# Performance work log

Hardware: AMD Instinct MI355X
Metric: run time of the kernel (lower is better)

Reference implementation:

```python
import jax, jax.numpy as jnp
import numpy as np

N_E, E_DIM = 1024, 256

def setup_inputs() -> dict:
    key = jax.random.key(0)
    k1, k2 = jax.random.split(key)
    z = jax.random.normal(k1, (16, E_DIM, 64, 64), dtype=jnp.float32)
    codebook = jax.random.normal(k2, (N_E, E_DIM), dtype=jnp.float32)
    return {"z": z, "codebook": codebook}

def reference(z, codebook):
    B, C, H, W = z.shape  # C == e_dim
    zp = jnp.transpose(z, (0, 2, 3, 1))          # B,H,W,C
    zf = zp.reshape(-1, C)                        # N,C with N=B*H*W
    # L2 distance: ||z||^2 + ||c||^2 - 2 z c^T  -> [N, n_e]
    d = (jnp.sum(zf * zf, axis=1, keepdims=True)
         + jnp.sum(codebook * codebook, axis=1)
         - 2.0 * jnp.matmul(zf, codebook.T))
    idx = jnp.argmin(d, axis=1)                   # [N] int
    # one-hot @ codebook == gather (same math)
    z_q = codebook[idx].reshape(zp.shape)         # B,H,W,C
    codebook_loss = jnp.mean((z_q - jax.lax.stop_gradient(zp)) ** 2)
    z_q_out = jnp.transpose(z_q, (0, 3, 1, 2))    # B,C,H,W
    min_encoding_indices = idx.reshape(B, 1, H, W)
    return (z_q_out, codebook_loss, jnp.zeros((), z_q_out.dtype), min_encoding_indices)
```

## Files before the change

kernel.cpp:

```cpp
#include <hip/hip_runtime.h>

#define HW 4096
#define NE 1024
#define LOSS_OFF 16777216
#define IDX_OFF  16777218
#define MARGIN 0.08f

typedef __attribute__((ext_vector_type(8))) _Float16 half8v;
typedef __attribute__((ext_vector_type(4))) float float4v;

#define WS_LIST_OFF   64
#define WS_CNORM_OFF  262208
#define WS_CBH_OFF    266304
#define WS_PART_OFF   790592

__device__ __forceinline__ unsigned short f16rne(float f) {
    _Float16 h = (_Float16)f;
    return __builtin_bit_cast(unsigned short, h);
}

__device__ __forceinline__ unsigned f16pk(float a, float b) {
    auto h = __builtin_amdgcn_cvt_pkrtz(a, b);
    return __builtin_bit_cast(unsigned, h);
}

__device__ __forceinline__ void stage16(const void* g, void* l) {
    __builtin_amdgcn_global_load_lds(
        (const __attribute__((address_space(1))) unsigned*)g,
        (__attribute__((address_space(3))) unsigned*)l, 16, 0, 0);
}

__global__ __launch_bounds__(256) void k0_prep(const float* __restrict__ cb,
                                               float* __restrict__ cnorm,
                                               unsigned short* __restrict__ cbh,
                                               int* __restrict__ flagcnt) {
    const int tid = threadIdx.x;
    if (blockIdx.x == 0 && tid == 0) *flagcnt = 0;
    const int e = blockIdx.x * 64 + (tid >> 2);
    const int j = tid & 3;
    const float4* src = (const float4*)(cb + (size_t)e * 256 + j * 64);
    unsigned short* dst = cbh + (size_t)e * 256 + j * 64;
    float s = 0.f;
#pragma unroll
    for (int i = 0; i < 16; ++i) {
        float4 v = src[i];
        s += v.x * v.x + v.y * v.y + v.z * v.z + v.w * v.w;
        unsigned p0 = (unsigned)f16rne(v.x) | ((unsigned)f16rne(v.y) << 16);
        unsigned p1 = (unsigned)f16rne(v.z) | ((unsigned)f16rne(v.w) << 16);
        *(uint2*)(dst + i * 4) = make_uint2(p0, p1);
    }
    s += __shfl_xor(s, 1, 64);
    s += __shfl_xor(s, 2, 64);
    if (j == 0) cnorm[e] = 0.5f * s;
}

__global__ __launch_bounds__(256) void k1_mfma(const float* __restrict__ z,
                                               const unsigned short* __restrict__ cbh,
                                               const float* __restrict__ cnorm,
                                               float* __restrict__ out_idx,
                                               int* __restrict__ flagcnt,
                                               int* __restrict__ flaglist) {
    __shared__ __align__(16) char smem[67072];
    float* cand1 = (float*)(smem + 65536);
    int*   candi = (int*)  (smem + 66048);
    float* cand2 = (float*)(smem + 66560);

    const int tid = threadIdx.x;
    const int lane = tid & 63, wid = tid >> 6;
    const int wx = wid & 1, wy = wid >> 1;
    const int lr = lane & 15, lg = lane >> 4;

    const int n0 = blockIdx.x * 64;
    const int hw0 = n0 & 4095;
    const float* zb = z + (size_t)(n0 >> 12) * (256 * HW);
    const char* cbh_b = (const char*)cbh;

    {
        const int row = tid & 63, kg8 = tid >> 6;
        const unsigned zswz = (unsigned)((row & 15) << 4);
#pragma unroll
        for (int it = 0; it < 8; ++it) {
            int kb = (kg8 + it * 4) * 8;
            float v[8];
#pragma unroll
            for (int q = 0; q < 8; ++q) v[q] = zb[(size_t)(kb + q) * HW + hw0 + row];
            unsigned pk[4];
#pragma unroll
            for (int q = 0; q < 4; ++q) pk[q] = f16pk(v[2*q], v[2*q+1]);
            unsigned scol = (unsigned)(kb * 2) ^ zswz;
            *(int4*)(smem + row * 512 + scol) = make_int4(pk[0], pk[1], pk[2], pk[3]);
        }
    }
    __syncthreads();

    half8v A[2][8];
#pragma unroll
    for (int mi = 0; mi < 2; ++mi)
#pragma unroll
        for (int ks = 0; ks < 8; ++ks)
            A[mi][ks] = *(const half8v*)(smem + (32*wy + 16*mi + lr) * 512
                                              + ((unsigned)(64*ks + 16*lg) ^ (unsigned)(lr << 4)));
    __syncthreads();

    char* mybuf0 = smem + wid * 8192;
    char* mybuf1 = smem + 32768 + wid * 8192;
    const int el      = (lane >> 5);
    const unsigned c0 = (unsigned)((lane & 31) * 16);
    const size_t  eb0 = (size_t)wx * 512;

#pragma unroll
    for (int i = 0; i < 8; ++i) {
        int e_loc = 2 * i + el;
        unsigned col = c0 ^ (unsigned)((e_loc & 15) << 4);
        stage16(cbh_b + (eb0 + e_loc) * 512 + col, mybuf0 + i * 1024);
    }

    const float* cnp = cnorm + wx * 512 + lr;
    float b1[8], b2[8]; int bi[8];
#pragma unroll
    for (int i = 0; i < 8; ++i) { b1[i] = 1e30f; b2[i] = 1e30f; bi[i] = 0; }

    for (int c = 0; c < 32; ++c) {
        char* cur = (c & 1) ? mybuf1 : mybuf0;
        if (c < 31) {
            char* nb = (c & 1) ? mybuf0 : mybuf1;
            const size_t ebase = eb0 + (size_t)(c + 1) * 16;
#pragma unroll
            for (int i = 0; i < 8; ++i) {
                int e_loc = 2 * i + el;
                unsigned col = c0 ^ (unsigned)((e_loc & 15) << 4);
                stage16(cbh_b + (ebase + e_loc) * 512 + col, nb + i * 1024);
            }
            asm volatile("s_waitcnt vmcnt(8)" ::: "memory");
        } else {
            asm volatile("s_waitcnt vmcnt(0)" ::: "memory");
        }
        __builtin_amdgcn_sched_barrier(0);

        const char* bp = cur + lr * 512;
        float4v a0 = {0.f,0.f,0.f,0.f}, a1 = a0;
#pragma unroll
        for (int ks = 0; ks < 8; ++ks) {
            half8v B = *(const half8v*)(bp + ((unsigned)(64*ks + 16*lg) ^ (unsigned)(lr << 4)));
            a0 = __builtin_amdgcn_mfma_f32_16x16x32_f16(A[0][ks], B, a0, 0, 0, 0);
            a1 = __builtin_amdgcn_mfma_f32_16x16x32_f16(A[1][ks], B, a1, 0, 0, 0);
        }

        const float cn = cnp[c * 16];
        const int e = wx * 512 + c * 16 + lr;
#pragma unroll
        for (int r = 0; r < 4; ++r) {
            float s0 = cn - a0[r];
            b2[r] = fminf(b2[r], fmaxf(b1[r], s0));
            if (s0 < b1[r]) { b1[r] = s0; bi[r] = e; }
            float s1 = cn - a1[r];
            b2[4+r] = fminf(b2[4+r], fmaxf(b1[4+r], s1));
            if (s1 < b1[4+r]) { b1[4+r] = s1; bi[4+r] = e; }
        }
    }

#pragma unroll
    for (int m = 1; m <= 8; m <<= 1) {
#pragma unroll
        for (int s = 0; s < 8; ++s) {
            float o1 = __shfl_xor(b1[s], m, 64);
            float o2 = __shfl_xor(b2[s], m, 64);
            int   oi = __shfl_xor(bi[s], m, 64);
            float m2 = fminf(fmaxf(b1[s], o1), fminf(b2[s], o2));
            if (o1 < b1[s] || (o1 == b1[s] && oi < bi[s])) { b1[s] = o1; bi[s] = oi; }
            b2[s] = m2;
        }
    }
    if (lr == 0) {
#pragma unroll
        for (int mi = 0; mi < 2; ++mi)
#pragma unroll
            for (int r = 0; r < 4; ++r) {
                int row = 32 * wy + 16 * mi + 4 * lg + r;
                cand1[row * 2 + wx] = b1[mi * 4 + r];
                cand2[row * 2 + wx] = b2[mi * 4 + r];
                candi[row * 2 + wx] = bi[mi * 4 + r];
            }
    }
    __syncthreads();
    if (tid < 64) {
        float s1a = cand1[tid * 2], s1b = cand1[tid * 2 + 1];
        int   ia = candi[tid * 2],  ib = candi[tid * 2 + 1];
        float s2 = fminf(fminf(cand2[tid * 2], cand2[tid * 2 + 1]), fmaxf(s1a, s1b));
        float s1; int iw;
        if (s1b < s1a || (s1b == s1a && ib < ia)) { s1 = s1b; iw = ib; }
        else { s1 = s1a; iw = ia; }
        out_idx[n0 + tid] = (float)iw;
        if (s2 - s1 < MARGIN) {
            int p = atomicAdd(flagcnt, 1);
            flaglist[p] = n0 + tid;
        }
    }
}

__global__ __launch_bounds__(256) void k1b_refine(const float* __restrict__ z,
                                                  const float* __restrict__ cb,
                                                  const float* __restrict__ cnorm,
                                                  const int* __restrict__ flagcnt,
                                                  const int* __restrict__ flaglist,
                                                  float* __restrict__ out_idx) {
    __shared__ float zr[4][260];
    __shared__ int   rows[4];
    __shared__ float wb[4][4];
    __shared__ int   wi[4][4];
    const int tid = threadIdx.x;
    const int lane = tid & 63, w = tid >> 6;
    const int gid = tid >> 2, j = tid & 3;
    const int count = *flagcnt;
    for (int base = blockIdx.x * 4; base < count; base += gridDim.x * 4) {
        const int nr = min(4, count - base);
        __syncthreads();
        if (tid < nr) rows[tid] = flaglist[base + tid];
        __syncthreads();
        for (int r = 0; r < nr; ++r) {
            const int n = rows[r];
            zr[r][tid] = z[((size_t)(n >> 12) * 256 + tid) * HW + (n & 4095)];
        }
        __syncthreads();

        float acc[16][4];
#pragma unroll
        for (int p = 0; p < 16; ++p)
#pragma unroll
            for (int r = 0; r < 4; ++r) acc[p][r] = 0.f;

        const char* cbase = (const char*)cb + (size_t)gid * 1024 + j * 16;
#pragma unroll 2
        for (int q = 0; q < 16; ++q) {
            float4 zv[4];
#pragma unroll
            for (int r = 0; r < 4; ++r) zv[r] = *(const float4*)(&zr[r][q * 16 + j * 4]);
#pragma unroll
            for (int p = 0; p < 16; ++p) {
                float4 c = *(const float4*)(cbase + (size_t)p * 65536 + q * 64);
#pragma unroll
                for (int r = 0; r < 4; ++r) {
                    float a = acc[p][r];
                    a = fmaf(zv[r].x, c.x, a);
                    a = fmaf(zv[r].y, c.y, a);
                    a = fmaf(zv[r].z, c.z, a);
                    a = fmaf(zv[r].w, c.w, a);
                    acc[p][r] = a;
                }
            }
        }

        float best[4]; int bidx[4];
#pragma unroll
        for (int r = 0; r < 4; ++r) { best[r] = 1e30f; bidx[r] = 0; }
#pragma unroll
        for (int p = 0; p < 16; ++p) {
            const int e = p * 64 + gid;
            const float cn = cnorm[e];
#pragma unroll
            for (int r = 0; r < 4; ++r) {
                float d = acc[p][r];
                d += __shfl_xor(d, 1, 64);
                d += __shfl_xor(d, 2, 64);
                float s = cn - d;
                if (s < best[r]) { best[r] = s; bidx[r] = e; }
            }
        }
#pragma unroll
        for (int m = 1; m <= 32; m <<= 1) {
#pragma unroll
            for (int r = 0; r < 4; ++r) {
                float ob = __shfl_xor(best[r], m, 64);
                int   oi = __shfl_xor(bidx[r], m, 64);
                if (ob < best[r] || (ob == best[r] && oi < bidx[r])) { best[r] = ob; bidx[r] = oi; }
            }
        }
        if (lane == 0) {
#pragma unroll
            for (int r = 0; r < 4; ++r) { wb[w][r] = best[r]; wi[w][r] = bidx[r]; }
        }
        __syncthreads();
        if (tid < nr) {
            float bb = wb[0][tid]; int ii = wi[0][tid];
#pragma unroll
            for (int q = 1; q < 4; ++q)
                if (wb[q][tid] < bb || (wb[q][tid] == bb && wi[q][tid] < ii)) { bb = wb[q][tid]; ii = wi[q][tid]; }
            out_idx[rows[tid]] = (float)ii;
        }
        __syncthreads();
    }
}

__global__ __launch_bounds__(256) void k2_scatter(const float* __restrict__ z,
                                                  const float* __restrict__ cb,
                                                  const float* __restrict__ idxf,
                                                  float* __restrict__ zq,
                                                  float* __restrict__ part) {
    __shared__ float cbrow[64][257];
    __shared__ int   earr[64];
    __shared__ float ls[4];
    const int tid = threadIdx.x;
    const int b = blockIdx.x >> 6;
    const int hw0 = (blockIdx.x & 63) * 64;

    if (tid < 64) earr[tid] = (int)idxf[b * 4096 + hw0 + tid];
    __syncthreads();
    {
        const int r = tid >> 2, qd = tid & 3;
        const float4* src = (const float4*)(cb + (size_t)earr[r] * 256 + qd * 64);
#pragma unroll
        for (int i = 0; i < 16; ++i) {
            float4 v = src[i];
            float* d = &cbrow[r][qd * 64 + i * 4];
            d[0] = v.x; d[1] = v.y; d[2] = v.z; d[3] = v.w;
        }
    }
    __syncthreads();

    const int hw = tid & 63, cq = tid >> 6;
    const size_t zbase = ((size_t)b * 256) * 4096 + hw0 + hw;
    float lsum = 0.f;
#pragma unroll 8
    for (int pass = 0; pass < 64; ++pass) {
        const int c = pass * 4 + cq;
        const size_t flat = zbase + (size_t)c * 4096;
        float q = cbrow[hw][c];
        zq[flat] = q;
        float d = q - z[flat];
        lsum = fmaf(d, d, lsum);
    }
#pragma unroll
    for (int m = 32; m >= 1; m >>= 1) lsum += __shfl_down(lsum, m, 64);
    const int lane = tid & 63, w = tid >> 6;
    if (lane == 0) ls[w] = lsum;
    __syncthreads();
    if (tid == 0) part[blockIdx.x] = ls[0] + ls[1] + ls[2] + ls[3];
}

__global__ __launch_bounds__(256) void k3_final(const float* __restrict__ part,
                                                float* __restrict__ dout) {
    __shared__ float ls[4];
    float s = 0.f;
#pragma unroll
    for (int it = 0; it < 4; ++it) s += part[threadIdx.x + it * 256];
#pragma unroll
    for (int m = 32; m >= 1; m >>= 1) s += __shfl_down(s, m, 64);
    int lane = threadIdx.x & 63, w = threadIdx.x >> 6;
    if (lane == 0) ls[w] = s;
    __syncthreads();
    if (threadIdx.x == 0) {
        float total = ls[0] + ls[1] + ls[2] + ls[3];
        dout[LOSS_OFF]     = total / 16777216.0f;
        dout[LOSS_OFF + 1] = 0.0f;
    }
}

extern "C" void kernel_launch(void* const* d_in, const int* in_sizes, int n_in,
                              void* d_out, int out_size, void* d_ws, size_t ws_size,
                              hipStream_t stream) {
    const float* z  = (const float*)d_in[0];
    const float* cb = (const float*)d_in[1];
    float* out = (float*)d_out;
    char* ws = (char*)d_ws;

    int*            flagcnt  = (int*)ws;
    int*            flaglist = (int*)(ws + WS_LIST_OFF);
    float*          cnorm    = (float*)(ws + WS_CNORM_OFF);
    unsigned short* cbh      = (unsigned short*)(ws + WS_CBH_OFF);
    float*          part     = (float*)(ws + WS_PART_OFF);

    hipLaunchKernelGGL(k0_prep,   dim3(16),   dim3(256), 0, stream, cb, cnorm, cbh, flagcnt);
    hipLaunchKernelGGL(k1_mfma,   dim3(1024), dim3(256), 0, stream,
                       z, cbh, cnorm, out + IDX_OFF, flagcnt, flaglist);
    hipLaunchKernelGGL(k1b_refine, dim3(2048), dim3(256), 0, stream,
                       z, cb, cnorm, flagcnt, flaglist, out + IDX_OFF);
    hipLaunchKernelGGL(k2_scatter, dim3(1024), dim3(256), 0, stream,
                       z, cb, out + IDX_OFF, out, part);
    hipLaunchKernelGGL(k3_final,  dim3(1),    dim3(256), 0, stream, part, out);
}
```

Measured before the change: 135.6 us.

## Retile VQ distance kernel: 2 waves each own 64 rows across full codebook

The MFMA distance kernel now uses 128-thread blocks covering 128 rows. Each wave holds 64 rows of z in registers and scans all 1024 codebook entries, instead of four waves splitting rows and codebook halves. Codebook tiles of 32 entries are staged cooperatively into shared double buffers with block-wide barriers, and the cross-wave candidate merge through shared memory is removed. This raises A-fragment reuse per B load and halves total codebook traffic per row, but it adds a barrier every iteration, roughly doubles register pressure for accumulators and top-2 state, and launches fewer, smaller blocks.

New measurement: 179.4 us. +32.3%, slower.

```diff
diff --git a/kernel.cpp b/kernel.cpp
--- a/kernel.cpp
+++ b/kernel.cpp
@@ -54,115 +54,119 @@
     if (j == 0) cnorm[e] = 0.5f * s;
 }
 
-__global__ __launch_bounds__(256) void k1_mfma(const float* __restrict__ z,
-                                               const unsigned short* __restrict__ cbh,
-                                               const float* __restrict__ cnorm,
-                                               float* __restrict__ out_idx,
-                                               int* __restrict__ flagcnt,
-                                               int* __restrict__ flaglist) {
-    __shared__ __align__(16) char smem[67072];
-    float* cand1 = (float*)(smem + 65536);
-    int*   candi = (int*)  (smem + 66048);
-    float* cand2 = (float*)(smem + 66560);
+__global__ __launch_bounds__(128, 2) void k1_mfma(const float* __restrict__ z,
+                                                  const unsigned short* __restrict__ cbh,
+                                                  const float* __restrict__ cnorm,
+                                                  float* __restrict__ out_idx,
+                                                  int* __restrict__ flagcnt,
+                                                  int* __restrict__ flaglist) {
+    __shared__ __align__(16) char smem[32768];
 
     const int tid = threadIdx.x;
-    const int lane = tid & 63, wid = tid >> 6;
-    const int wx = wid & 1, wy = wid >> 1;
+    const int lane = tid & 63, w = tid >> 6;
     const int lr = lane & 15, lg = lane >> 4;
-
-    const int n0 = blockIdx.x * 64;
+    const unsigned bswz = (unsigned)(lr << 4);
+
+    const int n0 = blockIdx.x * 128;
     const int hw0 = n0 & 4095;
     const float* zb = z + (size_t)(n0 >> 12) * (256 * HW);
     const char* cbh_b = (const char*)cbh;
 
-    {
+    half8v A[4][8];
+#pragma unroll
+    for (int h = 0; h < 2; ++h) {
         const int row = tid & 63, kg8 = tid >> 6;
         const unsigned zswz = (unsigned)((row & 15) << 4);
 #pragma unroll
-        for (int it = 0; it < 8; ++it) {
-            int kb = (kg8 + it * 4) * 8;
+        for (int it = 0; it < 16; ++it) {
+            int kb = (kg8 + it * 2) * 8;
             float v[8];
 #pragma unroll
-            for (int q = 0; q < 8; ++q) v[q] = zb[(size_t)(kb + q) * HW + hw0 + row];
+            for (int q = 0; q < 8; ++q)
+                v[q] = zb[(size_t)(kb + q) * HW + hw0 + 64 * h + row];
             unsigned pk[4];
 #pragma unroll
             for (int q = 0; q < 4; ++q) pk[q] = f16pk(v[2*q], v[2*q+1]);
-            unsigned scol = (unsigned)(kb * 2) ^ zswz;
-            *(int4*)(smem + row * 512 + scol) = make_int4(pk[0], pk[1], pk[2], pk[3]);
-        }
-    }
-    __syncthreads();
-
-    half8v A[2][8];
-#pragma unroll
-    for (int mi = 0; mi < 2; ++mi)
-#pragma unroll
-        for (int ks = 0; ks < 8; ++ks)
-            A[mi][ks] = *(const half8v*)(smem + (32*wy + 16*mi + lr) * 512
-                                              + ((unsigned)(64*ks + 16*lg) ^ (unsigned)(lr << 4)));
-    __syncthreads();
-
-    char* mybuf0 = smem + wid * 8192;
-    char* mybuf1 = smem + 32768 + wid * 8192;
-    const int el      = (lane >> 5);
+            *(int4*)(smem + row * 512 + ((unsigned)(kb * 2) ^ zswz)) =
+                make_int4(pk[0], pk[1], pk[2], pk[3]);
+        }
+        __syncthreads();
+        if (w == h) {
+#pragma unroll
+            for (int mi = 0; mi < 4; ++mi)
+#pragma unroll
+                for (int ks = 0; ks < 8; ++ks)
+                    A[mi][ks] = *(const half8v*)(smem + (16*mi + lr) * 512
+                                                      + ((unsigned)(64*ks + 16*lg) ^ bswz));
+        }
+        __syncthreads();
+    }
+
+    const int el = lane >> 5;
     const unsigned c0 = (unsigned)((lane & 31) * 16);
-    const size_t  eb0 = (size_t)wx * 512;
 
 #pragma unroll
     for (int i = 0; i < 8; ++i) {
-        int e_loc = 2 * i + el;
+        int e_loc = w * 16 + 2 * i + el;
         unsigned col = c0 ^ (unsigned)((e_loc & 15) << 4);
-        stage16(cbh_b + (eb0 + e_loc) * 512 + col, mybuf0 + i * 1024);
-    }
-
-    const float* cnp = cnorm + wx * 512 + lr;
-    float b1[8], b2[8]; int bi[8];
-#pragma unroll
-    for (int i = 0; i < 8; ++i) { b1[i] = 1e30f; b2[i] = 1e30f; bi[i] = 0; }
+        stage16(cbh_b + (size_t)e_loc * 512 + col, smem + (size_t)w * 8192 + i * 1024);
+    }
+    __syncthreads();
+
+    float b1[16], b2[16]; int bi[16];
+#pragma unroll
+    for (int i = 0; i < 16; ++i) { b1[i] = 1e30f; b2[i] = 1e30f; bi[i] = 0; }
 
     for (int c = 0; c < 32; ++c) {
-        char* cur = (c & 1) ? mybuf1 : mybuf0;
         if (c < 31) {
-            char* nb = (c & 1) ? mybuf0 : mybuf1;
-            const size_t ebase = eb0 + (size_t)(c + 1) * 16;
+            char* nb = smem + ((c + 1) & 1) * 16384 + w * 8192;
+            const size_t ebase = (size_t)(c + 1) * 32;
 #pragma unroll
             for (int i = 0; i < 8; ++i) {
-                int e_loc = 2 * i + el;
+                int e_loc = w * 16 + 2 * i + el;
                 unsigned col = c0 ^ (unsigned)((e_loc & 15) << 4);
                 stage16(cbh_b + (ebase + e_loc) * 512 + col, nb + i * 1024);
             }
-            asm volatile("s_waitcnt vmcnt(8)" ::: "memory");
-        } else {
-            asm volatile("s_waitcnt vmcnt(0)" ::: "memory");
-        }
-        __builtin_amdgcn_sched_barrier(0);
-
-        const char* bp = cur + lr * 512;
-        float4v a0 = {0.f,0.f,0.f,0.f}, a1 = a0;
-#pragma unroll
-        for (int ks = 0; ks < 8; ++ks) {
-            half8v B = *(const half8v*)(bp + ((unsigned)(64*ks + 16*lg) ^ (unsigned)(lr << 4)));
-            a0 = __builtin_amdgcn_mfma_f32_16x16x32_f16(A[0][ks], B, a0, 0, 0, 0);
-            a1 = __builtin_amdgcn_mfma_f32_16x16x32_f16(A[1][ks], B, a1, 0, 0, 0);
-        }
-
-        const float cn = cnp[c * 16];
-        const int e = wx * 512 + c * 16 + lr;
-#pragma unroll
-        for (int r = 0; r < 4; ++r) {
-            float s0 = cn - a0[r];
-            b2[r] = fminf(b2[r], fmaxf(b1[r], s0));
-            if (s0 < b1[r]) { b1[r] = s0; bi[r] = e; }
-            float s1 = cn - a1[r];
-            b2[4+r] = fminf(b2[4+r], fmaxf(b1[4+r], s1));
-            if (s1 < b1[4+r]) { b1[4+r] = s1; bi[4+r] = e; }
-        }
+        }
+
+        const char* bp = smem + (c & 1) * 16384;
+#pragma unroll
+        for (int jx = 0; jx < 2; ++jx) {
+            float4v acc0 = {0.f,0.f,0.f,0.f}, acc1 = acc0, acc2 = acc0, acc3 = acc0;
+            const char* brow = bp + (16 * jx + lr) * 512;
+#pragma unroll
+            for (int ks = 0; ks < 8; ++ks) {
+                half8v B = *(const half8v*)(brow + ((unsigned)(64*ks + 16*lg) ^ bswz));
+                acc0 = __builtin_amdgcn_mfma_f32_16x16x32_f16(A[0][ks], B, acc0, 0, 0, 0);
+                acc1 = __builtin_amdgcn_mfma_f32_16x16x32_f16(A[1][ks], B, acc1, 0, 0, 0);
+                acc2 = __builtin_amdgcn_mfma_f32_16x16x32_f16(A[2][ks], B, acc2, 0, 0, 0);
+                acc3 = __builtin_amdgcn_mfma_f32_16x16x32_f16(A[3][ks], B, acc3, 0, 0, 0);
+            }
+            const int e = c * 32 + 16 * jx + lr;
+            const float cn = cnorm[e];
+#pragma unroll
+            for (int r = 0; r < 4; ++r) {
+                float s0 = cn - acc0[r];
+                b2[r] = fminf(b2[r], fmaxf(b1[r], s0));
+                if (s0 < b1[r]) { b1[r] = s0; bi[r] = e; }
+                float s1 = cn - acc1[r];
+                b2[4+r] = fminf(b2[4+r], fmaxf(b1[4+r], s1));
+                if (s1 < b1[4+r]) { b1[4+r] = s1; bi[4+r] = e; }
+                float s2 = cn - acc2[r];
+                b2[8+r] = fminf(b2[8+r], fmaxf(b1[8+r], s2));
+                if (s2 < b1[8+r]) { b1[8+r] = s2; bi[8+r] = e; }
+                float s3 = cn - acc3[r];
+                b2[12+r] = fminf(b2[12+r], fmaxf(b1[12+r], s3));
+                if (s3 < b1[12+r]) { b1[12+r] = s3; bi[12+r] = e; }
+            }
+        }
+        __syncthreads();
     }
 
 #pragma unroll
     for (int m = 1; m <= 8; m <<= 1) {
 #pragma unroll
-        for (int s = 0; s < 8; ++s) {
+        for (int s = 0; s < 16; ++s) {
             float o1 = __shfl_xor(b1[s], m, 64);
             float o2 = __shfl_xor(b2[s], m, 64);
             int   oi = __shfl_xor(bi[s], m, 64);
@@ -173,28 +177,17 @@
     }
     if (lr == 0) {
 #pragma unroll
-        for (int mi = 0; mi < 2; ++mi)
+        for (int mi = 0; mi < 4; ++mi)
 #pragma unroll
             for (int r = 0; r < 4; ++r) {
-                int row = 32 * wy + 16 * mi + 4 * lg + r;
-                cand1[row * 2 + wx] = b1[mi * 4 + r];
-                cand2[row * 2 + wx] = b2[mi * 4 + r];
-                candi[row * 2 + wx] = bi[mi * 4 + r];
-            }
-    }
-    __syncthreads();
-    if (tid < 64) {
-        float s1a = cand1[tid * 2], s1b = cand1[tid * 2 + 1];
-        int   ia = candi[tid * 2],  ib = candi[tid * 2 + 1];
-        float s2 = fminf(fminf(cand2[tid * 2], cand2[tid * 2 + 1]), fmaxf(s1a, s1b));
-        float s1; int iw;
-        if (s1b < s1a || (s1b == s1a && ib < ia)) { s1 = s1b; iw = ib; }
-        else { s1 = s1a; iw = ia; }
-        out_idx[n0 + tid] = (float)iw;
-        if (s2 - s1 < MARGIN) {
-            int p = atomicAdd(flagcnt, 1);
-            flaglist[p] = n0 + tid;
-        }
+                const int s = mi * 4 + r;
+                const int rowg = n0 + 64 * w + 16 * mi + 4 * lg + r;
+                out_idx[rowg] = (float)bi[s];
+                if (b2[s] - b1[s] < MARGIN) {
+                    int p = atomicAdd(flagcnt, 1);
+                    flaglist[p] = rowg;
+                }
+            }
     }
 }
 
@@ -370,7 +363,7 @@
     float*          part     = (float*)(ws + WS_PART_OFF);
 
     hipLaunchKernelGGL(k0_prep,   dim3(16),   dim3(256), 0, stream, cb, cnorm, cbh, flagcnt);
-    hipLaunchKernelGGL(k1_mfma,   dim3(1024), dim3(256), 0, stream,
+    hipLaunchKernelGGL(k1_mfma,   dim3(512),  dim3(128), 0, stream,
                        z, cbh, cnorm, out + IDX_OFF, flagcnt, flaglist);
     hipLaunchKernelGGL(k1b_refine, dim3(2048), dim3(256), 0, stream,
                        z, cb, cnorm, flagcnt, flaglist, out + IDX_OFF);
```
